# Optimization experiments

Measured on AMD Instinct MI355X. Metric: run time of the kernel, lower is better.

Reference implementation:

```python
import jax, jax.numpy as jnp
import numpy as np

BN_EPS = 1e-5
BIND_CHAN = 4  # hparams.MODEL.LEARNABLE_OFFSET.BIND_CHAN


def conv1x1(x, w, b):
    # x: [B,C,H,W], w: [O,C], b: [O]
    return jnp.einsum('bchw,oc->bohw', x, w) + b[None, :, None, None]


def bn_train(x, gamma, beta):
    # training-mode batch norm over (B,H,W) per channel
    mean = jnp.mean(x, axis=(0, 2, 3), keepdims=True)
    var = jnp.var(x, axis=(0, 2, 3), keepdims=True)
    xn = (x - mean) * jax.lax.rsqrt(var + BN_EPS)
    return xn * gamma[None, :, None, None] + beta[None, :, None, None]


def displace_channel(x, offsets):
    # x: [B,C,H,W]; offsets: [C,2] (dy,dx) per channel, continuous.
    # out[b,c,y,x] = bilinear sample of x[b,c] at (y+dy_c, x+dx_c), zeros outside.
    B, C, H, W = x.shape
    dy, dx = offsets[:, 0], offsets[:, 1]
    fy, fx = jnp.floor(dy), jnp.floor(dx)
    wy, wx = dy - fy, dx - fx          # fractional weights, [C]
    iy, ix = fy.astype(jnp.int32), fx.astype(jnp.int32)
    chan = jnp.arange(C)[:, None, None]

    def shifted(oy, ox):
        ys = jnp.arange(H)[None, :] + oy[:, None]   # [C,H]
        xs = jnp.arange(W)[None, :] + ox[:, None]   # [C,W]
        valid = ((ys >= 0) & (ys < H))[:, :, None] & ((xs >= 0) & (xs < W))[:, None, :]
        ysc = jnp.clip(ys, 0, H - 1)
        xsc = jnp.clip(xs, 0, W - 1)
        g = x[:, chan, ysc[:, :, None], xsc[:, None, :]]   # [B,C,H,W]
        return g * valid.astype(x.dtype)[None]

    w00 = ((1 - wy) * (1 - wx))[None, :, None, None]
    w01 = ((1 - wy) * wx)[None, :, None, None]
    w10 = (wy * (1 - wx))[None, :, None, None]
    w11 = (wy * wx)[None, :, None, None]
    return (w00 * shifted(iy, ix) + w01 * shifted(iy, ix + 1)
            + w10 * shifted(iy + 1, ix) + w11 * shifted(iy + 1, ix + 1))


def setup_inputs() -> dict:
    key = jax.random.key(0)
    ks = jax.random.split(key, 12)
    B, Cin, H, W = 16, 64, 128, 128
    Cd, Cout = 128, 64
    n_off = Cd // BIND_CHAN  # 32
    s_in = 1.0 / np.sqrt(Cin)
    s_d = 1.0 / np.sqrt(Cd)
    return {
        'x': jax.random.normal(ks[0], (B, Cin, H, W), jnp.float32),
        'pre_w': jax.random.uniform(ks[1], (Cd, Cin), jnp.float32, -s_in, s_in),
        'pre_b': jax.random.uniform(ks[2], (Cd,), jnp.float32, -s_in, s_in),
        'post_w': jax.random.uniform(ks[3], (Cout, Cd), jnp.float32, -s_d, s_d),
        'post_b': jax.random.uniform(ks[4], (Cout,), jnp.float32, -s_d, s_d),
        'atten_w': jax.random.uniform(ks[5], (Cd, Cin), jnp.float32, -s_in, s_in),
        'atten_b': jax.random.uniform(ks[6], (Cd,), jnp.float32, -s_in, s_in),
        'atten_bn_g': jnp.ones((Cd,), jnp.float32),
        'atten_bn_b': jnp.zeros((Cd,), jnp.float32),
        'offsets': jax.random.normal(ks[7], (n_off, 2), jnp.float32) * 3.0,
        'bn_g': jnp.ones((Cout,), jnp.float32),
        'bn_b': jnp.zeros((Cout,), jnp.float32),
    }


def reference(x, pre_w, pre_b, post_w, post_b, atten_w, atten_b,
              atten_bn_g, atten_bn_b, offsets, bn_g, bn_b):
    # pre_offset conv1x1
    out_pre = conv1x1(x, pre_w, pre_b)                        # [B,Cd,H,W]
    # DisplaceChannel: each offset shared by BIND_CHAN consecutive channels
    off_per_chan = jnp.repeat(offsets, BIND_CHAN, axis=0)     # [Cd,2]
    out_dis = displace_channel(out_pre, off_per_chan)
    # Attention branch: conv1x1 -> BN -> Softplus -> SpaceNormalization
    a = conv1x1(x, atten_w, atten_b)
    a = bn_train(a, atten_bn_g, atten_bn_b)
    a = jax.nn.softplus(a)
    out_atten = a / jnp.sum(a, axis=(2, 3), keepdims=True)    # spatial normalization
    # post_offset conv1x1 on gated displaced features
    out_post = conv1x1(out_atten * out_dis, post_w, post_b)
    # residual (inplanes == outplanes, stride 1 -> no downsample) + BN + ReLU
    out_skip = x + out_post
    return jax.nn.relu(bn_train(out_skip, bn_g, bn_b))
```

## Files before the change

### kernel.cpp

```cpp
#include <hip/hip_runtime.h>

#define HWSZ   16384
#define CIN    64
#define CD     128
#define COUT   64
#define BN_EPS 1e-5f

typedef __attribute__((ext_vector_type(8))) short short8x;
typedef __attribute__((ext_vector_type(4))) float floatx4;

#define WS_ASTAT 25344
#define WS_OSTAT 25600
#define WS_BIG   32768
#define WS_TOTAL_BYTES ((size_t)(32768 + 16777216) * 4)

__device__ __forceinline__ unsigned short f2bf(float f) {
    unsigned int u = __float_as_uint(f);
    u += 0x7fff + ((u >> 16) & 1);
    return (unsigned short)(u >> 16);
}
__device__ __forceinline__ float bf2f(unsigned short s) {
    return __uint_as_float(((unsigned int)s) << 16);
}
__device__ __forceinline__ float softplus_fast(float x) {
    return fmaxf(x, 0.f) + __logf(1.f + __expf(-fabsf(x)));
}
__device__ __forceinline__ float block_reduce(float v, float* sc) {
    #pragma unroll
    for (int off = 32; off >= 1; off >>= 1) v += __shfl_xor(v, off, 64);
    int wv = threadIdx.x >> 6, ln = threadIdx.x & 63;
    int nw = blockDim.x >> 6;
    if (ln == 0) sc[wv] = v;
    __syncthreads();
    float r = ((int)threadIdx.x < nw) ? sc[threadIdx.x] : 0.f;
    r += __shfl_xor(r, 1, 64);
    r += __shfl_xor(r, 2, 64);
    r += __shfl_xor(r, 4, 64);
    return r;
}

__device__ __forceinline__ short8x cvt_w8(const float* src) {
    float4 f0 = *(const float4*)(src);
    float4 f1 = *(const float4*)(src + 4);
    short8x w;
    w[0] = (short)f2bf(f0.x); w[1] = (short)f2bf(f0.y);
    w[2] = (short)f2bf(f0.z); w[3] = (short)f2bf(f0.w);
    w[4] = (short)f2bf(f1.x); w[5] = (short)f2bf(f1.y);
    w[6] = (short)f2bf(f1.z); w[7] = (short)f2bf(f1.w);
    return w;
}

__device__ __forceinline__ void pre_write_lds(unsigned short* wbuf, int c, int wv,
                                              const float4 ld[4]) {
    #pragma unroll
    for (int k = 0; k < 4; ++k) {
        int px = wv * 16 + k * 4;
        wbuf[(px + 0) * 72 + c] = f2bf(ld[k].x);
        wbuf[(px + 1) * 72 + c] = f2bf(ld[k].y);
        wbuf[(px + 2) * 72 + c] = f2bf(ld[k].z);
        wbuf[(px + 3) * 72 + c] = f2bf(ld[k].w);
    }
}

__device__ __forceinline__ void pre_compute_tile(
        const unsigned short* buf, int ln, int o0, int b, int ptile,
        const short8x wfrag[4][2], const float4 biasv[4],
        unsigned short* __restrict__ out_pre, unsigned short* __restrict__ a_out) {
    floatx4 acc[4][4];
    #pragma unroll
    for (int oi = 0; oi < 4; ++oi)
        #pragma unroll
        for (int pi = 0; pi < 4; ++pi)
            acc[oi][pi] = floatx4{biasv[oi].x, biasv[oi].y, biasv[oi].z, biasv[oi].w};
    #pragma unroll
    for (int kk = 0; kk < 2; ++kk)
        #pragma unroll
        for (int pi = 0; pi < 4; ++pi) {
            short8x xfrag = *(const short8x*)((const char*)buf +
                    (pi * 16 + (ln & 15)) * 144 + (kk * 32 + (ln >> 4) * 8) * 2);
            #pragma unroll
            for (int oi = 0; oi < 4; ++oi)
                acc[oi][pi] = __builtin_amdgcn_mfma_f32_16x16x32_bf16(
                        wfrag[oi][kk], xfrag, acc[oi][pi], 0, 0, 0);
        }
    #pragma unroll
    for (int oi = 0; oi < 4; ++oi) {
        int og = o0 + oi * 16;
        unsigned short* dst = (og < 128) ? out_pre : a_out;
        int ob = (og < 128) ? og : og - 128;
        #pragma unroll
        for (int pi = 0; pi < 4; ++pi) {
            int px = ptile + pi * 16 + (ln & 15);
            #pragma unroll
            for (int r = 0; r < 4; ++r) {
                int o = ob + (ln >> 4) * 4 + r;
                dst[((size_t)b * CD + o) * HWSZ + px] = f2bf(acc[oi][pi][r]);
            }
        }
    }
}

__global__ __launch_bounds__(256) void conv_pre_mfma(
        const float* __restrict__ x, const float* __restrict__ pre_w,
        const float* __restrict__ atten_w,
        const float* __restrict__ pre_b, const float* __restrict__ atten_b,
        unsigned short* __restrict__ out_pre, unsigned short* __restrict__ a_out) {
    __shared__ unsigned short xT[2][64 * 72];
    int t = threadIdx.x;
    int wv = t >> 6, ln = t & 63;
    int b = blockIdx.x >> 6;
    int poff = (blockIdx.x & 63) << 8;
    const float* xg = x + (size_t)b * CIN * HWSZ + poff;
    int c = ln;

    int o0 = wv * 64;
    short8x wfrag[4][2];
    #pragma unroll
    for (int oi = 0; oi < 4; ++oi)
        #pragma unroll
        for (int kk = 0; kk < 2; ++kk) {
            int row = o0 + oi * 16 + (ln & 15);
            int kcol = kk * 32 + (ln >> 4) * 8;
            const float* wsrc = (row < 128) ? (pre_w + row * 64)
                                            : (atten_w + (row - 128) * 64);
            wfrag[oi][kk] = cvt_w8(wsrc + kcol);
        }
    float4 biasv[4];
    #pragma unroll
    for (int oi = 0; oi < 4; ++oi) {
        int og = o0 + oi * 16;
        const float* bias = (og < 128) ? (pre_b + og) : (atten_b + og - 128);
        biasv[oi] = *(const float4*)(bias + (ln >> 4) * 4);
    }

    float4 lda[4], ldb[4];
    #pragma unroll
    for (int k = 0; k < 4; ++k)
        lda[k] = *(const float4*)(xg + (size_t)c * HWSZ + 0 * 64 + wv * 16 + k * 4);
    pre_write_lds(xT[0], c, wv, lda);
    #pragma unroll
    for (int k = 0; k < 4; ++k)
        lda[k] = *(const float4*)(xg + (size_t)c * HWSZ + 1 * 64 + wv * 16 + k * 4);
    __syncthreads();

    #pragma unroll
    for (int k = 0; k < 4; ++k)
        ldb[k] = *(const float4*)(xg + (size_t)c * HWSZ + 2 * 64 + wv * 16 + k * 4);
    pre_compute_tile(xT[0], ln, o0, b, poff + 0 * 64, wfrag, biasv, out_pre, a_out);
    pre_write_lds(xT[1], c, wv, lda);
    __syncthreads();

    #pragma unroll
    for (int k = 0; k < 4; ++k)
        lda[k] = *(const float4*)(xg + (size_t)c * HWSZ + 3 * 64 + wv * 16 + k * 4);
    pre_compute_tile(xT[1], ln, o0, b, poff + 1 * 64, wfrag, biasv, out_pre, a_out);
    pre_write_lds(xT[0], c, wv, ldb);
    __syncthreads();

    pre_compute_tile(xT[0], ln, o0, b, poff + 2 * 64, wfrag, biasv, out_pre, a_out);
    pre_write_lds(xT[1], c, wv, lda);
    __syncthreads();

    pre_compute_tile(xT[1], ln, o0, b, poff + 3 * 64, wfrag, biasv, out_pre, a_out);
}

__global__ __launch_bounds__(256) void chan_stats_bf16(
        const unsigned short* __restrict__ src, float* __restrict__ stats) {
    __shared__ float sc1[8], sc2[8];
    int c = blockIdx.x, b = blockIdx.y;
    const unsigned short* base = src + ((size_t)b * CD + c) * HWSZ;
    int t = threadIdx.x;
    float sum = 0.f, sq = 0.f;
    #pragma unroll
    for (int i = 0; i < 8; ++i) {
        uint4 v = *(const uint4*)(base + i * 2048 + t * 8);
        unsigned int u[4] = {v.x, v.y, v.z, v.w};
        #pragma unroll
        for (int k = 0; k < 4; ++k) {
            float lo = bf2f((unsigned short)(u[k] & 0xffff));
            float hi = bf2f((unsigned short)(u[k] >> 16));
            sum += lo + hi;
            sq  += lo * lo + hi * hi;
        }
    }
    sum = block_reduce(sum, sc1);
    __syncthreads();
    sq = block_reduce(sq, sc2);
    if (t == 0) {
        atomicAdd(&stats[c * 2 + 0], sum);
        atomicAdd(&stats[c * 2 + 1], sq);
    }
}

struct Win9 { float v0,v1,v2,v3,v4,v5,v6,v7,v8; };
__device__ __forceinline__ Win9 extract9(uint4 qa, uint4 qb, bool s4, int sh) {
    unsigned long long A0 = ((unsigned long long)qa.y << 32) | qa.x;
    unsigned long long A1 = ((unsigned long long)qa.w << 32) | qa.z;
    unsigned long long A2 = ((unsigned long long)qb.y << 32) | qb.x;
    unsigned long long A3 = ((unsigned long long)qb.w << 32) | qb.z;
    unsigned long long B0 = s4 ? A1 : A0;
    unsigned long long B1 = s4 ? A2 : A1;
    unsigned long long B2 = s4 ? A3 : A2;
    unsigned long long r0 = sh ? ((B0 >> sh) | (B1 << (64 - sh))) : B0;
    unsigned long long r1 = sh ? ((B1 >> sh) | (B2 << (64 - sh))) : B1;
    unsigned int v8w = (unsigned int)(sh ? (B2 >> sh) : B2);
    Win9 w;
    w.v0 = bf2f((unsigned short)(r0 >>  0)); w.v1 = bf2f((unsigned short)(r0 >> 16));
    w.v2 = bf2f((unsigned short)(r0 >> 32)); w.v3 = bf2f((unsigned short)(r0 >> 48));
    w.v4 = bf2f((unsigned short)(r1 >>  0)); w.v5 = bf2f((unsigned short)(r1 >> 16));
    w.v6 = bf2f((unsigned short)(r1 >> 32)); w.v7 = bf2f((unsigned short)(r1 >> 48));
    w.v8 = bf2f((unsigned short)(v8w & 0xffff));
    return w;
}

__global__ __launch_bounds__(512) void displace_bnsp_gg(
        const unsigned short* __restrict__ pre, unsigned short* __restrict__ a_m,
        const float* __restrict__ stats, const float* __restrict__ g,
        const float* __restrict__ bb, const float* __restrict__ offsets) {
    __shared__ float sc[8];
    __shared__ float s_inv;
    int bc = blockIdx.x;
    int cc = bc & 127;
    float dy = offsets[(cc >> 2) * 2 + 0];
    float dx = offsets[(cc >> 2) * 2 + 1];
    float fy = floorf(dy), fx = floorf(dx);
    float wy = dy - fy, wx = dx - fx;
    int iy = (int)fy, ix = (int)fx;
    float w00 = (1.f - wy) * (1.f - wx);
    float w01 = (1.f - wy) * wx;
    float w10 = wy * (1.f - wx);
    float w11 = wy * wx;
    const float N = 262144.f;
    float mean = stats[cc * 2] / N;
    float var  = stats[cc * 2 + 1] / N - mean * mean;
    float rstd = rsqrtf(var + BN_EPS);
    float scl = rstd * g[cc];
    float shf = bb[cc] - mean * scl;
    const unsigned short* pg = pre + (size_t)bc * HWSZ;
    unsigned short* am = a_m + (size_t)bc * HWSZ;
    int t = threadIdx.x;
    uint4 aspr[4];
    float lsum = 0.f;
    #pragma unroll
    for (int i = 0; i < 4; ++i) {
        int px = i * 4096 + t * 8;
        uint4 av = *(const uint4*)(am + px);
        unsigned int au[4] = {av.x, av.y, av.z, av.w};
        unsigned int ou[4];
        #pragma unroll
        for (int k = 0; k < 4; ++k) {
            float lo = softplus_fast(bf2f((unsigned short)(au[k] & 0xffff)) * scl + shf);
            float hi = softplus_fast(bf2f((unsigned short)(au[k] >> 16))    * scl + shf);
            lsum += lo + hi;
            ou[k] = (unsigned int)f2bf(lo) | ((unsigned int)f2bf(hi) << 16);
        }
        aspr[i] = uint4{ou[0], ou[1], ou[2], ou[3]};
    }
    lsum = block_reduce(lsum, sc);
    if (t == 0) s_inv = 1.f / lsum;
    __syncthreads();
    float inv = s_inv;
    int s = ix & 7;
    int ix8 = ix - s;
    int sh = (s & 3) * 16;
    bool s4 = s >= 4;
    #pragma unroll
    for (int i = 0; i < 4; ++i) {
        int px = i * 4096 + t * 8;
        int y = px >> 7, x0 = px & 127;
        int yy0 = y + iy, yy1 = yy0 + 1;
        float wA0 = (yy0 >= 0 && yy0 < 128) ? w00 : 0.f;
        float wA1 = (yy0 >= 0 && yy0 < 128) ? w01 : 0.f;
        float wB0 = (yy1 >= 0 && yy1 < 128) ? w10 : 0.f;
        float wB1 = (yy1 >= 0 && yy1 < 128) ? w11 : 0.f;
        int yc0 = min(max(yy0, 0), 127), yc1 = min(max(yy1, 0), 127);
        int w0 = x0 + ix8;
        uint4 z = {0u, 0u, 0u, 0u};
        uint4 qa0 = (w0 >= 0 && w0 <= 120)         ? *(const uint4*)(pg + yc0 * 128 + w0)     : z;
        uint4 qa1 = (w0 + 8 >= 0 && w0 + 8 <= 120) ? *(const uint4*)(pg + yc0 * 128 + w0 + 8) : z;
        uint4 qb0 = (w0 >= 0 && w0 <= 120)         ? *(const uint4*)(pg + yc1 * 128 + w0)     : z;
        uint4 qb1 = (w0 + 8 >= 0 && w0 + 8 <= 120) ? *(const uint4*)(pg + yc1 * 128 + w0 + 8) : z;
        Win9 va = extract9(qa0, qa1, s4, sh);
        Win9 vb = extract9(qb0, qb1, s4, sh);
        float dv0 = wA0*va.v0 + wA1*va.v1 + wB0*vb.v0 + wB1*vb.v1;
        float dv1 = wA0*va.v1 + wA1*va.v2 + wB0*vb.v1 + wB1*vb.v2;
        float dv2 = wA0*va.v2 + wA1*va.v3 + wB0*vb.v2 + wB1*vb.v3;
        float dv3 = wA0*va.v3 + wA1*va.v4 + wB0*vb.v3 + wB1*vb.v4;
        float dv4 = wA0*va.v4 + wA1*va.v5 + wB0*vb.v4 + wB1*vb.v5;
        float dv5 = wA0*va.v5 + wA1*va.v6 + wB0*vb.v5 + wB1*vb.v6;
        float dv6 = wA0*va.v6 + wA1*va.v7 + wB0*vb.v6 + wB1*vb.v7;
        float dv7 = wA0*va.v7 + wA1*va.v8 + wB0*vb.v7 + wB1*vb.v8;
        unsigned int au[4] = {aspr[i].x, aspr[i].y, aspr[i].z, aspr[i].w};
        float a0 = bf2f((unsigned short)(au[0] & 0xffff)) * inv;
        float a1 = bf2f((unsigned short)(au[0] >> 16)) * inv;
        float a2 = bf2f((unsigned short)(au[1] & 0xffff)) * inv;
        float a3 = bf2f((unsigned short)(au[1] >> 16)) * inv;
        float a4 = bf2f((unsigned short)(au[2] & 0xffff)) * inv;
        float a5 = bf2f((unsigned short)(au[2] >> 16)) * inv;
        float a6 = bf2f((unsigned short)(au[3] & 0xffff)) * inv;
        float a7 = bf2f((unsigned short)(au[3] >> 16)) * inv;
        uint4 o;
        o.x = (unsigned int)f2bf(dv0 * a0) | ((unsigned int)f2bf(dv1 * a1) << 16);
        o.y = (unsigned int)f2bf(dv2 * a2) | ((unsigned int)f2bf(dv3 * a3) << 16);
        o.z = (unsigned int)f2bf(dv4 * a4) | ((unsigned int)f2bf(dv5 * a5) << 16);
        o.w = (unsigned int)f2bf(dv6 * a6) | ((unsigned int)f2bf(dv7 * a7) << 16);
        *(uint4*)(am + px) = o;
    }
}

__global__ __launch_bounds__(256) void conv_post_mfma(
        const unsigned short* __restrict__ m, const float* __restrict__ post_w,
        const float* __restrict__ post_b, const float* __restrict__ x,
        unsigned short* __restrict__ skipS) {
    __shared__ unsigned short mT[128 * 128];
    int t = threadIdx.x;
    int P0 = blockIdx.x * 128;
    int b = P0 >> 14, poff = P0 & 16383;
    int cl = t & 31, q = t >> 5;
    #pragma unroll
    for (int pass = 0; pass < 4; ++pass) {
        int c = cl + pass * 32;
        const unsigned short* mrow = m + ((size_t)b * CD + c) * HWSZ + poff;
        #pragma unroll
        for (int h = 0; h < 2; ++h) {
            int px0 = h * 64 + q * 8;
            uint4 v = *(const uint4*)(mrow + px0);
            unsigned int u[4] = {v.x, v.y, v.z, v.w};
            #pragma unroll
            for (int j = 0; j < 8; ++j) {
                unsigned short val = (unsigned short)((u[j >> 1] >> ((j & 1) * 16)) & 0xffff);
                int byteoff = (px0 + j) * 256 + ((c * 2) ^ (j << 4));
                *(unsigned short*)((char*)mT + byteoff) = val;
            }
        }
    }
    __syncthreads();
    int ln = t & 63, wv = t >> 6;
    int o0 = (wv >> 1) * 32;
    int ph = (wv & 1) * 64;
    short8x aw[2][4];
    #pragma unroll
    for (int oi = 0; oi < 2; ++oi)
        #pragma unroll
        for (int kk = 0; kk < 4; ++kk) {
            int o = o0 + oi * 16 + (ln & 15);
            aw[oi][kk] = cvt_w8(post_w + o * 128 + kk * 32 + (ln >> 4) * 8);
        }
    floatx4 acc[2][4];
    #pragma unroll
    for (int oi = 0; oi < 2; ++oi)
        #pragma unroll
        for (int pi = 0; pi < 4; ++pi) acc[oi][pi] = floatx4{0.f, 0.f, 0.f, 0.f};
    #pragma unroll
    for (int kk = 0; kk < 4; ++kk)
        #pragma unroll
        for (int pi = 0; pi < 4; ++pi) {
            int px = ph + pi * 16 + (ln & 15);
            int cb = kk * 64 + (ln >> 4) * 16;
            short8x bf = *(const short8x*)((const char*)mT + px * 256 + (cb ^ ((px & 7) << 4)));
            #pragma unroll
            for (int oi = 0; oi < 2; ++oi)
                acc[oi][pi] = __builtin_amdgcn_mfma_f32_16x16x32_bf16(aw[oi][kk], bf, acc[oi][pi], 0, 0, 0);
        }
    #pragma unroll
    for (int oi = 0; oi < 2; ++oi) {
        float4 b4 = *(const float4*)(post_b + o0 + oi * 16 + (ln >> 4) * 4);
        float bb[4] = {b4.x, b4.y, b4.z, b4.w};
        #pragma unroll
        for (int pi = 0; pi < 4; ++pi) {
            int pxg = poff + ph + pi * 16 + (ln & 15);
            #pragma unroll
            for (int r = 0; r < 4; ++r) {
                int o = o0 + oi * 16 + (ln >> 4) * 4 + r;
                float val = acc[oi][pi][r] + bb[r] + x[((size_t)b * COUT + o) * HWSZ + pxg];
                skipS[((size_t)b * CD + o) * HWSZ + pxg] = f2bf(val);
            }
        }
    }
}

__global__ __launch_bounds__(256) void bn_relu_out(
        const unsigned short* __restrict__ skipS, float* __restrict__ out,
        const float* __restrict__ stats, const float* __restrict__ g,
        const float* __restrict__ bb) {
    const float N = 262144.f;
    int t = threadIdx.x;
    #pragma unroll
    for (int k = 0; k < 4; ++k) {
        size_t gidx = (size_t)blockIdx.x * 1024 + k * 256 + t;
        size_t e = gidx * 8;
        int b = (int)(e >> 20);
        int c = (int)(e >> 14) & 63;
        int px = (int)(e & 16383);
        float mean = stats[c * 2] / N;
        float rstd = rsqrtf(stats[c * 2 + 1] / N - mean * mean + BN_EPS);
        float gc = g[c], bbc = bb[c];
        uint4 v = *(const uint4*)(skipS + ((size_t)b * CD + c) * HWSZ + px);
        unsigned int u[4] = {v.x, v.y, v.z, v.w};
        float4 o0, o1;
        float* op[8] = {&o0.x, &o0.y, &o0.z, &o0.w, &o1.x, &o1.y, &o1.z, &o1.w};
        #pragma unroll
        for (int j = 0; j < 8; ++j) {
            float val = bf2f((unsigned short)((u[j >> 1] >> ((j & 1) * 16)) & 0xffff));
            *op[j] = fmaxf((val - mean) * rstd * gc + bbc, 0.f);
        }
        *(float4*)(out + e) = o0;
        *(float4*)(out + e + 4) = o1;
    }
}

extern "C" void kernel_launch(void* const* d_in, const int* in_sizes, int n_in,
                              void* d_out, int out_size, void* d_ws, size_t ws_size,
                              hipStream_t stream) {
    const float* x          = (const float*)d_in[0];
    const float* pre_w      = (const float*)d_in[1];
    const float* pre_b      = (const float*)d_in[2];
    const float* post_w     = (const float*)d_in[3];
    const float* post_b     = (const float*)d_in[4];
    const float* atten_w    = (const float*)d_in[5];
    const float* atten_b    = (const float*)d_in[6];
    const float* atten_bn_g = (const float*)d_in[7];
    const float* atten_bn_b = (const float*)d_in[8];
    const float* offsets    = (const float*)d_in[9];
    const float* bn_g       = (const float*)d_in[10];
    const float* bn_b       = (const float*)d_in[11];
    float* out = (float*)d_out;
    float* ws  = (float*)d_ws;

    if (ws_size < WS_TOTAL_BYTES) return;

    float* a_stats = ws + WS_ASTAT;
    float* o_stats = ws + WS_OSTAT;
    unsigned short* big   = (unsigned short*)(ws + WS_BIG);
    unsigned short* a_buf = (unsigned short*)d_out;

    hipMemsetAsync((void*)a_stats, 0, 384 * sizeof(float), stream);

    conv_pre_mfma<<<1024, 256, 0, stream>>>(x, pre_w, atten_w, pre_b, atten_b, big, a_buf);
    chan_stats_bf16<<<dim3(128, 16), 256, 0, stream>>>(a_buf, a_stats);
    displace_bnsp_gg<<<2048, 512, 0, stream>>>(big, a_buf, a_stats, atten_bn_g, atten_bn_b, offsets);
    conv_post_mfma<<<2048, 256, 0, stream>>>(a_buf, post_w, post_b, x, big);
    chan_stats_bf16<<<dim3(64, 16), 256, 0, stream>>>(big, o_stats);
    bn_relu_out<<<2048, 256, 0, stream>>>(big, out, o_stats, bn_g, bn_b);
}
```

Before: 185.6 us.

## Stage conv_pre outputs through LDS for coalesced stores; stage displace image in LDS

conv_pre now swaps the MFMA operands so each lane holds consecutive pixels. It writes the tile to a padded LDS buffer, then issues 16-byte coalesced global stores per channel row instead of scattered 2-byte stores. The displace kernel copies the whole per-channel image into LDS and reads its bilinear taps from there rather than from global memory. It also writes its product in place over the pre buffer, which conv_post now reads. Costs are extra LDS capacity, which may lower occupancy, plus additional barriers.

```diff
diff --git a/kernel.cpp b/kernel.cpp
--- a/kernel.cpp
+++ b/kernel.cpp
@@ -50,6 +50,8 @@
     return w;
 }
 
+#define OBPAD 68
+
 __device__ __forceinline__ void pre_write_lds(unsigned short* wbuf, int c, int wv,
                                               const float4 ld[4]) {
     #pragma unroll
@@ -63,15 +65,14 @@
 }
 
 __device__ __forceinline__ void pre_compute_tile(
-        const unsigned short* buf, int ln, int o0, int b, int ptile,
-        const short8x wfrag[4][2], const float4 biasv[4],
-        unsigned short* __restrict__ out_pre, unsigned short* __restrict__ a_out) {
+        const unsigned short* buf, unsigned short* ob, int ln, int wv,
+        const short8x wfrag[4][2], const float bv[4]) {
     floatx4 acc[4][4];
     #pragma unroll
     for (int oi = 0; oi < 4; ++oi)
         #pragma unroll
         for (int pi = 0; pi < 4; ++pi)
-            acc[oi][pi] = floatx4{biasv[oi].x, biasv[oi].y, biasv[oi].z, biasv[oi].w};
+            acc[oi][pi] = floatx4{bv[oi], bv[oi], bv[oi], bv[oi]};
     #pragma unroll
     for (int kk = 0; kk < 2; ++kk)
         #pragma unroll
@@ -81,21 +82,18 @@
             #pragma unroll
             for (int oi = 0; oi < 4; ++oi)
                 acc[oi][pi] = __builtin_amdgcn_mfma_f32_16x16x32_bf16(
-                        wfrag[oi][kk], xfrag, acc[oi][pi], 0, 0, 0);
+                        xfrag, wfrag[oi][kk], acc[oi][pi], 0, 0, 0);
         }
     #pragma unroll
     for (int oi = 0; oi < 4; ++oi) {
-        int og = o0 + oi * 16;
-        unsigned short* dst = (og < 128) ? out_pre : a_out;
-        int ob = (og < 128) ? og : og - 128;
+        int row = wv * 64 + oi * 16 + (ln & 15);
         #pragma unroll
         for (int pi = 0; pi < 4; ++pi) {
-            int px = ptile + pi * 16 + (ln & 15);
-            #pragma unroll
-            for (int r = 0; r < 4; ++r) {
-                int o = ob + (ln >> 4) * 4 + r;
-                dst[((size_t)b * CD + o) * HWSZ + px] = f2bf(acc[oi][pi][r]);
-            }
+            int px = pi * 16 + (ln >> 4) * 4;
+            ushort4 v;
+            v.x = f2bf(acc[oi][pi][0]); v.y = f2bf(acc[oi][pi][1]);
+            v.z = f2bf(acc[oi][pi][2]); v.w = f2bf(acc[oi][pi][3]);
+            *(ushort4*)&ob[row * OBPAD + px] = v;
         }
     }
 }
@@ -106,6 +104,7 @@
         const float* __restrict__ pre_b, const float* __restrict__ atten_b,
         unsigned short* __restrict__ out_pre, unsigned short* __restrict__ a_out) {
     __shared__ unsigned short xT[2][64 * 72];
+    __shared__ unsigned short ob[256 * OBPAD];
     int t = threadIdx.x;
     int wv = t >> 6, ln = t & 63;
     int b = blockIdx.x >> 6;
@@ -125,12 +124,11 @@
                                             : (atten_w + (row - 128) * 64);
             wfrag[oi][kk] = cvt_w8(wsrc + kcol);
         }
-    float4 biasv[4];
+    float bv[4];
     #pragma unroll
     for (int oi = 0; oi < 4; ++oi) {
         int og = o0 + oi * 16;
-        const float* bias = (og < 128) ? (pre_b + og) : (atten_b + og - 128);
-        biasv[oi] = *(const float4*)(bias + (ln >> 4) * 4);
+        bv[oi] = (og < 128) ? pre_b[og + (ln & 15)] : atten_b[og - 128 + (ln & 15)];
     }
 
     float4 lda[4], ldb[4];
@@ -144,24 +142,33 @@
     __syncthreads();
 
     #pragma unroll
-    for (int k = 0; k < 4; ++k)
-        ldb[k] = *(const float4*)(xg + (size_t)c * HWSZ + 2 * 64 + wv * 16 + k * 4);
-    pre_compute_tile(xT[0], ln, o0, b, poff + 0 * 64, wfrag, biasv, out_pre, a_out);
-    pre_write_lds(xT[1], c, wv, lda);
-    __syncthreads();
-
-    #pragma unroll
-    for (int k = 0; k < 4; ++k)
-        lda[k] = *(const float4*)(xg + (size_t)c * HWSZ + 3 * 64 + wv * 16 + k * 4);
-    pre_compute_tile(xT[1], ln, o0, b, poff + 1 * 64, wfrag, biasv, out_pre, a_out);
-    pre_write_lds(xT[0], c, wv, ldb);
-    __syncthreads();
-
-    pre_compute_tile(xT[0], ln, o0, b, poff + 2 * 64, wfrag, biasv, out_pre, a_out);
-    pre_write_lds(xT[1], c, wv, lda);
-    __syncthreads();
-
-    pre_compute_tile(xT[1], ln, o0, b, poff + 3 * 64, wfrag, biasv, out_pre, a_out);
+    for (int tt = 0; tt < 4; ++tt) {
+        if (tt == 0) {
+            #pragma unroll
+            for (int k = 0; k < 4; ++k)
+                ldb[k] = *(const float4*)(xg + (size_t)c * HWSZ + 2 * 64 + wv * 16 + k * 4);
+        } else if (tt == 1) {
+            #pragma unroll
+            for (int k = 0; k < 4; ++k)
+                lda[k] = *(const float4*)(xg + (size_t)c * HWSZ + 3 * 64 + wv * 16 + k * 4);
+        }
+        pre_compute_tile(xT[tt & 1], ob, ln, wv, wfrag, bv);
+        if (tt == 0)      pre_write_lds(xT[1], c, wv, lda);
+        else if (tt == 1) pre_write_lds(xT[0], c, wv, ldb);
+        else if (tt == 2) pre_write_lds(xT[1], c, wv, lda);
+        __syncthreads();
+        int ptile = poff + tt * 64;
+        #pragma unroll
+        for (int j = 0; j < 8; ++j) {
+            int row = j * 32 + (t >> 3);
+            int px  = (t & 7) * 8;
+            uint4 v = *(const uint4*)&ob[row * OBPAD + px];
+            unsigned short* dst = (row < 128) ? out_pre : a_out;
+            int o = row & 127;
+            *(uint4*)(dst + ((size_t)b * CD + o) * HWSZ + ptile + px) = v;
+        }
+        __syncthreads();
+    }
 }
 
 __global__ __launch_bounds__(256) void chan_stats_bf16(
@@ -213,10 +220,11 @@
     return w;
 }
 
-__global__ __launch_bounds__(512) void displace_bnsp_gg(
-        const unsigned short* __restrict__ pre, unsigned short* __restrict__ a_m,
+__global__ __launch_bounds__(512) void displace_bnsp_mul(
+        unsigned short* __restrict__ pre, const unsigned short* __restrict__ a_raw,
         const float* __restrict__ stats, const float* __restrict__ g,
         const float* __restrict__ bb, const float* __restrict__ offsets) {
+    __shared__ unsigned short img[128 * 136];
     __shared__ float sc[8];
     __shared__ float s_inv;
     int bc = blockIdx.x;
@@ -236,15 +244,18 @@
     float rstd = rsqrtf(var + BN_EPS);
     float scl = rstd * g[cc];
     float shf = bb[cc] - mean * scl;
-    const unsigned short* pg = pre + (size_t)bc * HWSZ;
-    unsigned short* am = a_m + (size_t)bc * HWSZ;
+    unsigned short* pb = pre + (size_t)bc * HWSZ;
+    const unsigned short* ab = a_raw + (size_t)bc * HWSZ;
     int t = threadIdx.x;
     uint4 aspr[4];
     float lsum = 0.f;
     #pragma unroll
     for (int i = 0; i < 4; ++i) {
         int px = i * 4096 + t * 8;
-        uint4 av = *(const uint4*)(am + px);
+        uint4 v = *(const uint4*)(pb + px);
+        int y = px >> 7, xx = px & 127;
+        *(uint4*)&img[y * 136 + xx] = v;
+        uint4 av = *(const uint4*)(ab + px);
         unsigned int au[4] = {av.x, av.y, av.z, av.w};
         unsigned int ou[4];
         #pragma unroll
@@ -276,10 +287,10 @@
         int yc0 = min(max(yy0, 0), 127), yc1 = min(max(yy1, 0), 127);
         int w0 = x0 + ix8;
         uint4 z = {0u, 0u, 0u, 0u};
-        uint4 qa0 = (w0 >= 0 && w0 <= 120)         ? *(const uint4*)(pg + yc0 * 128 + w0)     : z;
-        uint4 qa1 = (w0 + 8 >= 0 && w0 + 8 <= 120) ? *(const uint4*)(pg + yc0 * 128 + w0 + 8) : z;
-        uint4 qb0 = (w0 >= 0 && w0 <= 120)         ? *(const uint4*)(pg + yc1 * 128 + w0)     : z;
-        uint4 qb1 = (w0 + 8 >= 0 && w0 + 8 <= 120) ? *(const uint4*)(pg + yc1 * 128 + w0 + 8) : z;
+        uint4 qa0 = (w0 >= 0 && w0 <= 120)         ? *(const uint4*)&img[yc0 * 136 + w0]     : z;
+        uint4 qa1 = (w0 + 8 >= 0 && w0 + 8 <= 120) ? *(const uint4*)&img[yc0 * 136 + w0 + 8] : z;
+        uint4 qb0 = (w0 >= 0 && w0 <= 120)         ? *(const uint4*)&img[yc1 * 136 + w0]     : z;
+        uint4 qb1 = (w0 + 8 >= 0 && w0 + 8 <= 120) ? *(const uint4*)&img[yc1 * 136 + w0 + 8] : z;
         Win9 va = extract9(qa0, qa1, s4, sh);
         Win9 vb = extract9(qb0, qb1, s4, sh);
         float dv0 = wA0*va.v0 + wA1*va.v1 + wB0*vb.v0 + wB1*vb.v1;
@@ -304,7 +315,7 @@
         o.y = (unsigned int)f2bf(dv2 * a2) | ((unsigned int)f2bf(dv3 * a3) << 16);
         o.z = (unsigned int)f2bf(dv4 * a4) | ((unsigned int)f2bf(dv5 * a5) << 16);
         o.w = (unsigned int)f2bf(dv6 * a6) | ((unsigned int)f2bf(dv7 * a7) << 16);
-        *(uint4*)(am + px) = o;
+        *(uint4*)(pb + px) = o;
     }
 }
 
@@ -438,8 +449,8 @@
 
     conv_pre_mfma<<<1024, 256, 0, stream>>>(x, pre_w, atten_w, pre_b, atten_b, big, a_buf);
     chan_stats_bf16<<<dim3(128, 16), 256, 0, stream>>>(a_buf, a_stats);
-    displace_bnsp_gg<<<2048, 512, 0, stream>>>(big, a_buf, a_stats, atten_bn_g, atten_bn_b, offsets);
-    conv_post_mfma<<<2048, 256, 0, stream>>>(a_buf, post_w, post_b, x, big);
+    displace_bnsp_mul<<<2048, 512, 0, stream>>>(big, a_buf, a_stats, atten_bn_g, atten_bn_b, offsets);
+    conv_post_mfma<<<2048, 256, 0, stream>>>(big, post_w, post_b, x, big);
     chan_stats_bf16<<<dim3(64, 16), 256, 0, stream>>>(big, o_stats);
     bn_relu_out<<<2048, 256, 0, stream>>>(big, out, o_stats, bn_g, bn_b);
 }
```

Result: faster. 164.2 us (-11.6%).
